# Kernel tuning notes

Measured on AMD Instinct MI355X. Metric: run time of the kernel, lower is better.

Reference implementation:

```python
import math
import jax, jax.numpy as jnp
import numpy as np

N_VARS = 10
K_MAX = 2
D = 32
B = 262144


def _fourier_emb(t, k_max=K_MAX):
    # [B, 1 + 2*k_max]: [1, cos(w t), sin(w t), cos(2 w t), sin(2 w t)]
    omega = 2.0 * math.pi
    feats = [jnp.ones_like(t)]
    for k in range(1, k_max + 1):
        feats.append(jnp.cos(k * omega * t))
        feats.append(jnp.sin(k * omega * t))
    return jnp.stack(feats, axis=-1)


def _make_mask(n_vars=N_VARS, mask_mode='th_only'):
    mask = jnp.eye(n_vars, dtype=jnp.float32)
    if mask_mode == 'th_only':
        mask = mask.at[:, 0].set(1.0)
        mask = mask.at[:, 1].set(1.0)
    else:
        mask = jnp.ones((n_vars, n_vars), dtype=jnp.float32)
    return mask


def setup_inputs() -> dict:
    key = jax.random.key(0)
    ks = jax.random.split(key, 8)
    x = jax.random.normal(ks[0], (B, N_VARS), dtype=jnp.float32)
    t_years = jax.random.uniform(ks[1], (B,), dtype=jnp.float32)
    n_basis = 1 + 2 * K_MAX
    # xavier-uniform-ish init for L_basis (fan over last two dims)
    limit = math.sqrt(6.0 / (N_VARS + N_VARS))
    L_basis = jax.random.uniform(ks[2], (n_basis, N_VARS, N_VARS), dtype=jnp.float32,
                                 minval=-limit, maxval=limit)
    wq = jax.random.normal(ks[3], (D,), dtype=jnp.float32)
    wk = jax.random.normal(ks[4], (D,), dtype=jnp.float32)
    wv = jax.random.normal(ks[5], (D,), dtype=jnp.float32)
    wo = jax.random.normal(ks[6], (D,), dtype=jnp.float32)
    alpha_w = 0.1 * jax.random.normal(ks[7], (n_basis,), dtype=jnp.float32)
    return {"x": x, "t_years": t_years, "L_basis": L_basis,
            "wq": wq, "wk": wk, "wv": wv, "wo": wo, "alpha_w": alpha_w}


def reference(x, t_years, L_basis, wq, wk, wv, wo, alpha_w):
    emb = _fourier_emb(t_years)                       # [B, K]
    L_t = jnp.einsum('bk,kuv->buv', emb, L_basis)      # [B, V, V]
    dxdt = jnp.einsum('buv,bv->bu', L_t, x)            # [B, V]

    # tokens: x[..., None] with Linear(1, d, bias=False) == outer product with weight vector
    Q = x[..., None] * wq                              # [B, V, D]
    K = x[..., None] * wk
    Vv = x[..., None] * wv

    scale = 1.0 / math.sqrt(D)
    scores = jnp.einsum('bvd,bud->bvu', Q, K) * scale  # [B, V, V]
    mask = _make_mask()
    scores = jnp.where(mask[None] < 0.5, -1e9, scores)
    attn = jax.nn.softmax(scores, axis=-1)
    O = jnp.einsum('bvu,bud->bvd', attn, Vv)           # [B, V, D]
    out = jnp.einsum('bvd,d->bv', O, wo)               # Wo: Linear(d,1,bias=False)

    alpha = jax.nn.sigmoid(emb @ alpha_w)              # [B]
    return dxdt + out * alpha[:, None]
```

## Files before the change

kernel.cpp:

```cpp
#include <hip/hip_runtime.h>
#include <math.h>

constexpr int NV  = 10;
constexpr int BLK = 256;

#define CONST_AS __attribute__((address_space(4)))
__device__ __forceinline__ const CONST_AS float* cptr(const float* p) {
    return (const CONST_AS float*)(unsigned long long)p;
}

template<int H>
__device__ __forceinline__ void dxdt_half(const float4* __restrict__ L4,
                                          const float emb[5], const float xv[NV],
                                          float dx[5]) {
    #pragma unroll
    for (int k = 0; k < 5; ++k) {
        float zv[NV];
        const float ek = emb[k];
        #pragma unroll
        for (int v = 0; v < NV; ++v)
            zv[v] = (k == 0) ? xv[v] : ek * xv[v];
        #pragma unroll
        for (int j = 0; j < 13; ++j) {
            const int qi = 25 * k + 12 * H + j;
            const float4 q = L4[qi];
            #pragma unroll
            for (int cc = 0; cc < 4; ++cc) {
                const int ed    = 4 * qi + cc;
                const int local = ed - (100 * k + 50 * H);
                if (local >= 0 && local < 50) {
                    const int u = local / 10;
                    const int v = local % 10;
                    const float qc = (cc == 0) ? q.x : (cc == 1) ? q.y
                                   : (cc == 2) ? q.z : q.w;
                    dx[u] = fmaf(qc, zv[v], dx[u]);
                }
            }
        }
    }
}

template<int H>
__device__ __forceinline__ void attn_half(const float xv[NV], const float dx[5],
                                          float c, float ga, float res[5]) {
    const float x0 = xv[0], x1 = xv[1];
    #pragma unroll
    for (int i = 0; i < 5; ++i) {
        const int v = 5 * H + i;
        const float s0 = xv[v] * x0 * c;
        const float s1 = xv[v] * x1 * c;
        float w;
        if (v < 2) {
            const float m = fmaxf(s0, s1);
            const float e0 = __expf(s0 - m), e1 = __expf(s1 - m);
            w = fmaf(e0, x0, e1 * x1) * __builtin_amdgcn_rcpf(e0 + e1);
        } else {
            const float sv = xv[v] * xv[v] * c;
            const float m = fmaxf(fmaxf(s0, s1), sv);
            const float e0 = __expf(s0 - m), e1 = __expf(s1 - m),
                        ev = __expf(sv - m);
            w = fmaf(e0, x0, fmaf(e1, x1, ev * xv[v]))
                * __builtin_amdgcn_rcpf(e0 + e1 + ev);
        }
        res[i] = fmaf(w, ga, dx[i]);
    }
}

__global__ __launch_bounds__(BLK, 8) void nxro_fused(
    const float* __restrict__ x,
    const float* __restrict__ t,
    const float* __restrict__ L,
    const float* __restrict__ wq,
    const float* __restrict__ wk,
    const float* __restrict__ wv,
    const float* __restrict__ wo,
    const float* __restrict__ aw,
    float* __restrict__ out,
    int B)
{
    const int tid  = threadIdx.x;
    const int lane = tid & 63;
    const int rloc = tid & 127;
    const int h    = tid >> 7;

    const long long row = (long long)blockIdx.x * 128 + rloc;
    const bool act = (row < (long long)B);
    const long long ri = act ? row : 0;

    const float tt = t[ri];
    float2 p[5];
    {
        const float2* xr = reinterpret_cast<const float2*>(x + ri * NV);
        #pragma unroll
        for (int i = 0; i < 5; ++i) p[i] = xr[i];
    }

    float pa, pb;
    if (lane < 32) { pa = wq[lane];      pb = wk[lane];      }
    else           { pa = wv[lane - 32]; pb = wo[lane - 32]; }
    float dotv = pa * pb;
    #pragma unroll
    for (int m = 16; m >= 1; m >>= 1)
        dotv += __shfl_xor(dotv, m, 64);
    const float c = __shfl(dotv, 0, 64) * 0.17677669529663687f;
    const float g = __shfl(dotv, 32, 64);

    const float t2 = tt + tt;
    const float emb[5] = {
        1.f,
        __builtin_amdgcn_cosf(tt),
        __builtin_amdgcn_sinf(tt),
        __builtin_amdgcn_cosf(t2),
        __builtin_amdgcn_sinf(t2)
    };

    float xv[NV];
    #pragma unroll
    for (int i = 0; i < 5; ++i) { xv[2*i] = p[i].x; xv[2*i+1] = p[i].y; }

    const CONST_AS float* awc = cptr(aw);
    float zs = awc[0];
    zs = fmaf(emb[1], awc[1], zs);
    zs = fmaf(emb[2], awc[2], zs);
    zs = fmaf(emb[3], awc[3], zs);
    zs = fmaf(emb[4], awc[4], zs);
    const float ga = g * __builtin_amdgcn_rcpf(1.f + __expf(-zs));

    const float4* __restrict__ L4 = reinterpret_cast<const float4*>(L);
    float dx[5] = {0.f, 0.f, 0.f, 0.f, 0.f};
    float res[5];

    if (h == 0) {
        dxdt_half<0>(L4, emb, xv, dx);
        attn_half<0>(xv, dx, c, ga, res);
        if (act) {
            float* op = out + row * NV;
            *reinterpret_cast<float2*>(op)     = make_float2(res[0], res[1]);
            *reinterpret_cast<float2*>(op + 2) = make_float2(res[2], res[3]);
            op[4] = res[4];
        }
    } else {
        dxdt_half<1>(L4, emb, xv, dx);
        attn_half<1>(xv, dx, c, ga, res);
        if (act) {
            float* op = out + row * NV + 5;
            op[0] = res[0];
            *reinterpret_cast<float2*>(op + 1) = make_float2(res[1], res[2]);
            *reinterpret_cast<float2*>(op + 3) = make_float2(res[3], res[4]);
        }
    }
}

extern "C" void kernel_launch(void* const* d_in, const int* in_sizes, int n_in,
                              void* d_out, int out_size, void* d_ws, size_t ws_size,
                              hipStream_t stream) {
    const float* x  = (const float*)d_in[0];
    const float* t  = (const float*)d_in[1];
    const float* L  = (const float*)d_in[2];
    const float* wq = (const float*)d_in[3];
    const float* wk = (const float*)d_in[4];
    const float* wv = (const float*)d_in[5];
    const float* wo = (const float*)d_in[6];
    const float* aw = (const float*)d_in[7];
    float* out = (float*)d_out;
    const int B = in_sizes[1];

    const int rowsPerBlk = 128;
    const int grid = (B + rowsPerBlk - 1) / rowsPerBlk;
    nxro_fused<<<grid, BLK, 0, stream>>>(x, t, L, wq, wk, wv, wo, aw, out, B);
}
```

Measured before the change: 13.06 us.

## Stage x loads and output stores through LDS for coalesced float4 access

Each block now loads its contiguous 128-row tile of x with coalesced float4 reads into padded shared memory, then threads read their row from LDS. Results are written to a padded shared buffer and stored back with coalesced float4 writes. This replaces strided per-thread float2 loads and stores, which were poorly coalesced and read each row twice across the two half-block groups. It adds two barriers and about 11 KB of LDS per block, which may limit occupancy.

After: 38.35 us. 2.94x slower.

```diff
diff --git a/kernel.cpp b/kernel.cpp
--- a/kernel.cpp
+++ b/kernel.cpp
@@ -1,8 +1,11 @@
 #include <hip/hip_runtime.h>
 #include <math.h>
 
-constexpr int NV  = 10;
-constexpr int BLK = 256;
+constexpr int NV   = 10;
+constexpr int BLK  = 256;
+constexpr int RPB  = 128;
+constexpr int LP   = 11;
+constexpr int TQ   = RPB * NV / 4;
 
 #define CONST_AS __attribute__((address_space(4)))
 __device__ __forceinline__ const CONST_AS float* cptr(const float* p) {
@@ -78,22 +81,35 @@
     float* __restrict__ out,
     int B)
 {
+    __shared__ float sx[RPB * LP];
+    __shared__ float so[RPB * LP];
+
     const int tid  = threadIdx.x;
     const int lane = tid & 63;
     const int rloc = tid & 127;
     const int h    = tid >> 7;
 
-    const long long row = (long long)blockIdx.x * 128 + rloc;
+    const long long base = (long long)blockIdx.x * RPB;
+    const long long row  = base + rloc;
     const bool act = (row < (long long)B);
     const long long ri = act ? row : 0;
 
+    {
+        const float4* xg4 = reinterpret_cast<const float4*>(x + base * NV);
+        const long long lim4 = ((long long)B * NV - base * NV) / 4;
+        #pragma unroll
+        for (int q = tid; q < TQ; q += BLK) {
+            const float4 val = (q < lim4) ? xg4[q]
+                                          : make_float4(0.f, 0.f, 0.f, 0.f);
+            const int e0 = 4 * q;
+            sx[(e0    ) / NV * LP + (e0    ) % NV] = val.x;
+            sx[(e0 + 1) / NV * LP + (e0 + 1) % NV] = val.y;
+            sx[(e0 + 2) / NV * LP + (e0 + 2) % NV] = val.z;
+            sx[(e0 + 3) / NV * LP + (e0 + 3) % NV] = val.w;
+        }
+    }
+
     const float tt = t[ri];
-    float2 p[5];
-    {
-        const float2* xr = reinterpret_cast<const float2*>(x + ri * NV);
-        #pragma unroll
-        for (int i = 0; i < 5; ++i) p[i] = xr[i];
-    }
 
     float pa, pb;
     if (lane < 32) { pa = wq[lane];      pb = wk[lane];      }
@@ -114,9 +130,11 @@
         __builtin_amdgcn_sinf(t2)
     };
 
+    __syncthreads();
+
     float xv[NV];
     #pragma unroll
-    for (int i = 0; i < 5; ++i) { xv[2*i] = p[i].x; xv[2*i+1] = p[i].y; }
+    for (int v = 0; v < NV; ++v) xv[v] = sx[rloc * LP + v];
 
     const CONST_AS float* awc = cptr(aw);
     float zs = awc[0];
@@ -133,20 +151,31 @@
     if (h == 0) {
         dxdt_half<0>(L4, emb, xv, dx);
         attn_half<0>(xv, dx, c, ga, res);
-        if (act) {
-            float* op = out + row * NV;
-            *reinterpret_cast<float2*>(op)     = make_float2(res[0], res[1]);
-            *reinterpret_cast<float2*>(op + 2) = make_float2(res[2], res[3]);
-            op[4] = res[4];
-        }
+        #pragma unroll
+        for (int i = 0; i < 5; ++i) so[rloc * LP + i] = res[i];
     } else {
         dxdt_half<1>(L4, emb, xv, dx);
         attn_half<1>(xv, dx, c, ga, res);
-        if (act) {
-            float* op = out + row * NV + 5;
-            op[0] = res[0];
-            *reinterpret_cast<float2*>(op + 1) = make_float2(res[1], res[2]);
-            *reinterpret_cast<float2*>(op + 3) = make_float2(res[3], res[4]);
+        #pragma unroll
+        for (int i = 0; i < 5; ++i) so[rloc * LP + 5 + i] = res[i];
+    }
+
+    __syncthreads();
+
+    {
+        float4* og4 = reinterpret_cast<float4*>(out + base * NV);
+        const long long lim4 = ((long long)B * NV - base * NV) / 4;
+        #pragma unroll
+        for (int q = tid; q < TQ; q += BLK) {
+            if (q < lim4) {
+                const int e0 = 4 * q;
+                float4 val;
+                val.x = so[(e0    ) / NV * LP + (e0    ) % NV];
+                val.y = so[(e0 + 1) / NV * LP + (e0 + 1) % NV];
+                val.z = so[(e0 + 2) / NV * LP + (e0 + 2) % NV];
+                val.w = so[(e0 + 3) / NV * LP + (e0 + 3) % NV];
+                og4[q] = val;
+            }
         }
     }
 }
@@ -165,7 +194,6 @@
     float* out = (float*)d_out;
     const int B = in_sizes[1];
 
-    const int rowsPerBlk = 128;
-    const int grid = (B + rowsPerBlk - 1) / rowsPerBlk;
+    const int grid = (B + RPB - 1) / RPB;
     nxro_fused<<<grid, BLK, 0, stream>>>(x, t, L, wq, wk, wv, wo, aw, out, B);
 }
```
